# Optimization experiments

Hardware: AMD Instinct MI355X
Metric: run time of the kernel (lower is better)

The kernel has to match this reference:

```python
import jax, jax.numpy as jnp
import numpy as np

DK = 64

def setup_inputs() -> dict:
    key = jax.random.key(0)
    kx, kq, kk, kv = jax.random.split(key, 4)
    B, T, DM, DV = 256, 256, 384, 64
    x = jax.random.normal(kx, (B, T, DM), dtype=jnp.float32)
    s = 1.0 / np.sqrt(DM)
    W_q = jax.random.normal(kq, (DM, DK), dtype=jnp.float32) * s
    W_k = jax.random.normal(kk, (DM, DK), dtype=jnp.float32) * s
    W_v = jax.random.normal(kv, (DM, DV), dtype=jnp.float32) * s
    return {"x": x, "W_q": W_q, "W_k": W_k, "W_v": W_v}

def reference(x, W_q, W_k, W_v):
    # x: [B, T, dm]; projections to [B, T, dk]/[B, T, dv]
    q = jnp.einsum('btc,ck->btk', x, W_q)
    k = jnp.einsum('btc,ck->btk', x, W_k)
    v = jnp.einsum('btc,cv->btv', x, W_v)
    scale = k.shape[-1] ** (-0.5)
    wei = jnp.einsum('btk,bsk->bts', q, k) * scale  # [B, T, T]
    T = x.shape[1]
    causal = jnp.tril(jnp.ones((T, T), dtype=bool))
    wei = jnp.where(causal, wei, -jnp.inf)
    wei = jax.nn.softmax(wei, axis=-1)
    # dropout omitted (eval mode / deterministic reference)
    out = jnp.einsum('bts,bsv->btv', wei, v)
    return out
```

## Files before the change

### kernel.cpp

```cpp
#include <hip/hip_runtime.h>


typedef __attribute__((ext_vector_type(8))) short short8;
typedef __attribute__((ext_vector_type(4))) float floatx4;

__device__ inline unsigned short f2bf(float f) {
  union { float f; unsigned u; } v; v.f = f;
  unsigned r = v.u + 0x7FFFu + ((v.u >> 16) & 1u);
  return (unsigned short)(r >> 16);
}

__device__ inline void glds16(const void* g, void* l) {
  __builtin_amdgcn_global_load_lds(
      (const __attribute__((address_space(1))) void*)g,
      (__attribute__((address_space(3))) void*)l, 16, 0, 0);
}

__global__ void wt_kernel(const float* __restrict__ wq, const float* __restrict__ wk,
                          const float* __restrict__ wv, unsigned short* __restrict__ wt) {
  int idx = blockIdx.x * 256 + threadIdx.x;
  if (idx >= 3 * 64 * 384) return;
  int mat = idx / (64 * 384);
  int rem = idx % (64 * 384);
  int n = rem / 384, k = rem % 384;
  const float* w = (mat == 0) ? wq : ((mat == 1) ? wk : wv);
  wt[idx] = f2bf(w[k * 64 + n]);
}

__global__ __launch_bounds__(1024) void fused_kernel(
    const float* __restrict__ x, const unsigned short* __restrict__ wt,
    float* __restrict__ out) {
  __shared__ __align__(16) unsigned short wb[2][3 * 192 * 32];
  __shared__ __align__(16) unsigned short sK[256 * 72];
  __shared__ __align__(16) unsigned short sVT[64 * 264];

  int tid = threadIdx.x, lane = tid & 63, w = tid >> 6;
  int m = lane & 15, q = lane >> 4;
  int b = blockIdx.x;
  const float* xb = x + (size_t)b * 256 * 384;

  auto stage = [&](int mega, int buf) {
#pragma unroll
    for (int t = 0; t < 3; ++t) {
      int i = w + 16 * t;
      if (i < 36) {
        int kc = i / 12, sub = i % 12;
        int c = sub * 16 + (lane >> 2), g = lane & 3;
        glds16(wt + (size_t)c * 384 + (mega * 3 + kc) * 32 + g * 8,
               (void*)&wb[buf][kc * 6144 + sub * 512]);
      }
    }
  };

  floatx4 z = {0.f, 0.f, 0.f, 0.f};
  floatx4 acc[12];
#pragma unroll
  for (int nt = 0; nt < 12; ++nt) acc[nt] = z;

  stage(0, 0);
#pragma unroll
  for (int mega = 0; mega < 4; ++mega) {
    int buf = mega & 1;
    __syncthreads();
    if (mega < 3) stage(mega + 1, buf ^ 1);

#pragma unroll
    for (int kc = 0; kc < 3; ++kc) {
      int ks = mega * 3 + kc;
      const float* ap = xb + (size_t)(w * 16 + m) * 384 + ks * 32 + q * 8;
      float4 f0 = *(const float4*)ap;
      float4 f1 = *(const float4*)(ap + 4);
      short8 af;
      af[0] = (short)f2bf(f0.x); af[1] = (short)f2bf(f0.y);
      af[2] = (short)f2bf(f0.z); af[3] = (short)f2bf(f0.w);
      af[4] = (short)f2bf(f1.x); af[5] = (short)f2bf(f1.y);
      af[6] = (short)f2bf(f1.z); af[7] = (short)f2bf(f1.w);

      const unsigned short* wbk = &wb[buf][kc * 6144];
#pragma unroll
      for (int nt = 0; nt < 12; ++nt) {
        short8 bf = *(const short8*)&wbk[(nt * 16 + m) * 32 + q * 8];
        acc[nt] = __builtin_amdgcn_mfma_f32_16x16x32_bf16(af, bf, acc[nt], 0, 0, 0);
      }
    }
  }

  unsigned short* scr = &wb[0][0] + w * 1152;
#pragma unroll
  for (int nt = 0; nt < 8; ++nt) {
#pragma unroll
    for (int j = 0; j < 4; ++j) {
      unsigned short val = f2bf(acc[nt][j]);
      int lrow = q * 4 + j;
      if (nt < 4) scr[lrow * 72 + nt * 16 + m] = val;
      else        sK[(w * 16 + lrow) * 72 + (nt - 4) * 16 + m] = val;
    }
  }
#pragma unroll
  for (int nt = 8; nt < 12; ++nt) {
    ushort4 pv;
    pv.x = f2bf(acc[nt][0]); pv.y = f2bf(acc[nt][1]);
    pv.z = f2bf(acc[nt][2]); pv.w = f2bf(acc[nt][3]);
    *(ushort4*)&sVT[((nt - 8) * 16 + m) * 264 + w * 16 + q * 4] = pv;
  }

  short8 qf0 = *(const short8*)(scr + m * 72 + q * 8);
  short8 qf1 = *(const short8*)(scr + m * 72 + 32 + q * 8);

  __syncthreads();

  floatx4 sacc[16];
#pragma unroll
  for (int nt = 0; nt < 16; ++nt) {
    if (nt > w) continue;
    short8 kb0 = *(const short8*)(sK + (nt * 16 + m) * 72 + q * 8);
    short8 kb1 = *(const short8*)(sK + (nt * 16 + m) * 72 + 32 + q * 8);
    floatx4 t = __builtin_amdgcn_mfma_f32_16x16x32_bf16(qf0, kb0, z, 0, 0, 0);
    sacc[nt] = __builtin_amdgcn_mfma_f32_16x16x32_bf16(qf1, kb1, t, 0, 0, 0);
  }

  const float CSC = 0.18033688011112042f;
  float inv_[4];
  int rbase = w * 16 + q * 4;
#pragma unroll
  for (int j = 0; j < 4; ++j) {
    int rg = rbase + j;
    float sum = 0.f;
#pragma unroll
    for (int nt = 0; nt < 16; ++nt) {
      if (nt > w) continue;
      int col = nt * 16 + m;
      float p = (col <= rg) ? exp2f(sacc[nt][j] * CSC) : 0.f;
      sacc[nt][j] = p;
      sum += p;
    }
    sum += __shfl_xor(sum, 1);
    sum += __shfl_xor(sum, 2);
    sum += __shfl_xor(sum, 4);
    sum += __shfl_xor(sum, 8);
    inv_[j] = 1.f / sum;
  }

  floatx4 o[4];
#pragma unroll
  for (int vt = 0; vt < 4; ++vt) o[vt] = z;
#pragma unroll
  for (int c = 0; c < 4; ++c) {
    if (4 * c > w) continue;
#pragma unroll
    for (int t = 0; t < 4; ++t) {
      int nt = 4 * c + t;
#pragma unroll
      for (int j = 0; j < 4; ++j) {
        unsigned short pv = (nt <= w) ? f2bf(sacc[nt][j] * inv_[j]) : (unsigned short)0;
        scr[(q * 4 + j) * 72 + t * 16 + m] = pv;
      }
    }
    short8 pf0 = *(const short8*)(scr + m * 72 + q * 8);
    short8 pf1 = *(const short8*)(scr + m * 72 + 32 + q * 8);
#pragma unroll
    for (int vt = 0; vt < 4; ++vt) {
      short8 vb0 = *(const short8*)(sVT + (vt * 16 + m) * 264 + c * 64 + q * 8);
      short8 vb1 = *(const short8*)(sVT + (vt * 16 + m) * 264 + c * 64 + 32 + q * 8);
      o[vt] = __builtin_amdgcn_mfma_f32_16x16x32_bf16(pf0, vb0, o[vt], 0, 0, 0);
      o[vt] = __builtin_amdgcn_mfma_f32_16x16x32_bf16(pf1, vb1, o[vt], 0, 0, 0);
    }
  }

  float* op = out + ((size_t)b * 256 + w * 16) * 64;
#pragma unroll
  for (int vt = 0; vt < 4; ++vt)
#pragma unroll
    for (int j = 0; j < 4; ++j)
      op[(q * 4 + j) * 64 + vt * 16 + m] = o[vt][j];
}

extern "C" void kernel_launch(void* const* d_in, const int* in_sizes, int n_in,
                              void* d_out, int out_size, void* d_ws, size_t ws_size,
                              hipStream_t stream) {
  const float* x  = (const float*)d_in[0];
  const float* wq = (const float*)d_in[1];
  const float* wk = (const float*)d_in[2];
  const float* wv = (const float*)d_in[3];
  float* out = (float*)d_out;

  unsigned short* wt = (unsigned short*)d_ws;

  wt_kernel<<<288, 256, 0, stream>>>(wq, wk, wv, wt);
  fused_kernel<<<256, 1024, 0, stream>>>(x, wt, out);
}
```

Measured before the change: 170.8 us.

## Load all projection weights to LDS once and tile projection 2x6 per wave

The projection GEMM now stages the whole bf16 weight matrix (144KB) into LDS in a single pass, replacing the double-buffered staging with a sync per mega-step. Each wave computes a 32-row by 96-column tile instead of 16x192, so each weight fragment read from LDS feeds two MFMAs. The weight layout in LDS is XOR-swizzled to reduce bank conflicts. The x loads are software-prefetched one k-step ahead, and bf16 conversion uses packed intrinsics. Q now goes through a dedicated LDS region. The trade-off is a large LDS footprint and an upfront load that exposes the full weight fetch latency before any compute starts.

Result: slower. 176.2 us (+3.2%).

```diff
diff --git a/kernel.cpp b/kernel.cpp
--- a/kernel.cpp
+++ b/kernel.cpp
@@ -1,4 +1,5 @@
 #include <hip/hip_runtime.h>
+#include <hip/hip_bf16.h>
 
 
 typedef __attribute__((ext_vector_type(8))) short short8;
@@ -8,6 +9,11 @@
   union { float f; unsigned u; } v; v.f = f;
   unsigned r = v.u + 0x7FFFu + ((v.u >> 16) & 1u);
   return (unsigned short)(r >> 16);
+}
+__device__ inline unsigned pk2bf(float lo, float hi) {
+  __hip_bfloat162 h = __float22bfloat162_rn(make_float2(lo, hi));
+  union { __hip_bfloat162 h; unsigned u; } c; c.h = h;
+  return c.u;
 }
 
 __device__ inline void glds16(const void* g, void* l) {
@@ -30,85 +36,100 @@
 __global__ __launch_bounds__(1024) void fused_kernel(
     const float* __restrict__ x, const unsigned short* __restrict__ wt,
     float* __restrict__ out) {
-  __shared__ __align__(16) unsigned short wb[2][3 * 192 * 32];
-  __shared__ __align__(16) unsigned short sK[256 * 72];
-  __shared__ __align__(16) unsigned short sVT[64 * 264];
+  __shared__ __align__(16) unsigned char lds[147456];
+  unsigned short* wtl = (unsigned short*)lds;
+  unsigned short* sK  = (unsigned short*)lds;
+  unsigned short* sVT = (unsigned short*)(lds + 36864);
+  unsigned short* sQ  = (unsigned short*)(lds + 70656);
+  unsigned short* scrA = (unsigned short*)(lds + 107520);
 
   int tid = threadIdx.x, lane = tid & 63, w = tid >> 6;
   int m = lane & 15, q = lane >> 4;
+  int rg = w >> 1, cg = w & 1;
   int b = blockIdx.x;
   const float* xb = x + (size_t)b * 256 * 384;
 
-  auto stage = [&](int mega, int buf) {
-#pragma unroll
-    for (int t = 0; t < 3; ++t) {
-      int i = w + 16 * t;
-      if (i < 36) {
-        int kc = i / 12, sub = i % 12;
-        int c = sub * 16 + (lane >> 2), g = lane & 3;
-        glds16(wt + (size_t)c * 384 + (mega * 3 + kc) * 32 + g * 8,
-               (void*)&wb[buf][kc * 6144 + sub * 512]);
+#pragma unroll
+  for (int t = 0; t < 9; ++t) {
+    int i = w * 9 + t;
+    int chunk = i / 12, sub = i % 12;
+    int c = sub * 16 + (lane >> 2);
+    int g = (lane & 3) ^ (c & 3);
+    glds16(wt + (size_t)c * 384 + chunk * 32 + g * 8,
+           (void*)(wtl + i * 512));
+  }
+
+  const float* arow0 = xb + (size_t)(32 * rg + m) * 384 + q * 8;
+  const float* arow1 = arow0 + 16 * 384;
+  float4 c00 = *(const float4*)arow0, c01 = *(const float4*)(arow0 + 4);
+  float4 c10 = *(const float4*)arow1, c11 = *(const float4*)(arow1 + 4);
+
+  floatx4 z = {0.f, 0.f, 0.f, 0.f};
+  floatx4 acc[2][6];
+#pragma unroll
+  for (int a = 0; a < 2; ++a)
+#pragma unroll
+    for (int n = 0; n < 6; ++n) acc[a][n] = z;
+
+  __syncthreads();
+
+#pragma unroll 1
+  for (int ks = 0; ks < 12; ++ks) {
+    float4 n00, n01, n10, n11;
+    if (ks < 11) {
+      n00 = *(const float4*)(arow0 + (ks + 1) * 32);
+      n01 = *(const float4*)(arow0 + (ks + 1) * 32 + 4);
+      n10 = *(const float4*)(arow1 + (ks + 1) * 32);
+      n11 = *(const float4*)(arow1 + (ks + 1) * 32 + 4);
+    }
+    short8 af[2];
+    {
+      union { short8 s; unsigned u[4]; } t0, t1;
+      t0.u[0] = pk2bf(c00.x, c00.y); t0.u[1] = pk2bf(c00.z, c00.w);
+      t0.u[2] = pk2bf(c01.x, c01.y); t0.u[3] = pk2bf(c01.z, c01.w);
+      t1.u[0] = pk2bf(c10.x, c10.y); t1.u[1] = pk2bf(c10.z, c10.w);
+      t1.u[2] = pk2bf(c11.x, c11.y); t1.u[3] = pk2bf(c11.z, c11.w);
+      af[0] = t0.s; af[1] = t1.s;
+    }
+    const unsigned short* wck = wtl + ks * 6144;
+#pragma unroll
+    for (int nt = 0; nt < 6; ++nt) {
+      int c = cg * 96 + nt * 16 + m;
+      short8 bf = *(const short8*)&wck[c * 32 + (q ^ (m & 3)) * 8];
+      acc[0][nt] = __builtin_amdgcn_mfma_f32_16x16x32_bf16(af[0], bf, acc[0][nt], 0, 0, 0);
+      acc[1][nt] = __builtin_amdgcn_mfma_f32_16x16x32_bf16(af[1], bf, acc[1][nt], 0, 0, 0);
+    }
+    c00 = n00; c01 = n01; c10 = n10; c11 = n11;
+  }
+
+  __syncthreads();
+
+#pragma unroll
+  for (int mt = 0; mt < 2; ++mt) {
+    int rowb = 32 * rg + mt * 16 + q * 4;
+#pragma unroll
+    for (int nt = 0; nt < 6; ++nt) {
+      int cb = cg * 96 + nt * 16;
+      if (cb < 128) {
+#pragma unroll
+        for (int j = 0; j < 4; ++j) {
+          unsigned short val = f2bf(acc[mt][nt][j]);
+          if (cb < 64) sQ[(rowb + j) * 72 + cb + m]      = val;
+          else         sK[(rowb + j) * 72 + cb - 64 + m] = val;
+        }
+      } else {
+        ushort4 pv;
+        pv.x = f2bf(acc[mt][nt][0]); pv.y = f2bf(acc[mt][nt][1]);
+        pv.z = f2bf(acc[mt][nt][2]); pv.w = f2bf(acc[mt][nt][3]);
+        *(ushort4*)&sVT[(cb - 128 + m) * 264 + rowb] = pv;
       }
     }
-  };
-
-  floatx4 z = {0.f, 0.f, 0.f, 0.f};
-  floatx4 acc[12];
-#pragma unroll
-  for (int nt = 0; nt < 12; ++nt) acc[nt] = z;
-
-  stage(0, 0);
-#pragma unroll
-  for (int mega = 0; mega < 4; ++mega) {
-    int buf = mega & 1;
-    __syncthreads();
-    if (mega < 3) stage(mega + 1, buf ^ 1);
-
-#pragma unroll
-    for (int kc = 0; kc < 3; ++kc) {
-      int ks = mega * 3 + kc;
-      const float* ap = xb + (size_t)(w * 16 + m) * 384 + ks * 32 + q * 8;
-      float4 f0 = *(const float4*)ap;
-      float4 f1 = *(const float4*)(ap + 4);
-      short8 af;
-      af[0] = (short)f2bf(f0.x); af[1] = (short)f2bf(f0.y);
-      af[2] = (short)f2bf(f0.z); af[3] = (short)f2bf(f0.w);
-      af[4] = (short)f2bf(f1.x); af[5] = (short)f2bf(f1.y);
-      af[6] = (short)f2bf(f1.z); af[7] = (short)f2bf(f1.w);
-
-      const unsigned short* wbk = &wb[buf][kc * 6144];
-#pragma unroll
-      for (int nt = 0; nt < 12; ++nt) {
-        short8 bf = *(const short8*)&wbk[(nt * 16 + m) * 32 + q * 8];
-        acc[nt] = __builtin_amdgcn_mfma_f32_16x16x32_bf16(af, bf, acc[nt], 0, 0, 0);
-      }
-    }
-  }
-
-  unsigned short* scr = &wb[0][0] + w * 1152;
-#pragma unroll
-  for (int nt = 0; nt < 8; ++nt) {
-#pragma unroll
-    for (int j = 0; j < 4; ++j) {
-      unsigned short val = f2bf(acc[nt][j]);
-      int lrow = q * 4 + j;
-      if (nt < 4) scr[lrow * 72 + nt * 16 + m] = val;
-      else        sK[(w * 16 + lrow) * 72 + (nt - 4) * 16 + m] = val;
-    }
-  }
-#pragma unroll
-  for (int nt = 8; nt < 12; ++nt) {
-    ushort4 pv;
-    pv.x = f2bf(acc[nt][0]); pv.y = f2bf(acc[nt][1]);
-    pv.z = f2bf(acc[nt][2]); pv.w = f2bf(acc[nt][3]);
-    *(ushort4*)&sVT[((nt - 8) * 16 + m) * 264 + w * 16 + q * 4] = pv;
-  }
-
-  short8 qf0 = *(const short8*)(scr + m * 72 + q * 8);
-  short8 qf1 = *(const short8*)(scr + m * 72 + 32 + q * 8);
+  }
 
   __syncthreads();
 
+  short8 qf0 = *(const short8*)(sQ + (w * 16 + m) * 72 + q * 8);
+  short8 qf1 = *(const short8*)(sQ + (w * 16 + m) * 72 + 32 + q * 8);
   floatx4 sacc[16];
 #pragma unroll
   for (int nt = 0; nt < 16; ++nt) {
@@ -124,13 +145,13 @@
   int rbase = w * 16 + q * 4;
 #pragma unroll
   for (int j = 0; j < 4; ++j) {
-    int rg = rbase + j;
+    int rgl = rbase + j;
     float sum = 0.f;
 #pragma unroll
     for (int nt = 0; nt < 16; ++nt) {
       if (nt > w) continue;
       int col = nt * 16 + m;
-      float p = (col <= rg) ? exp2f(sacc[nt][j] * CSC) : 0.f;
+      float p = (col <= rgl) ? exp2f(sacc[nt][j] * CSC) : 0.f;
       sacc[nt][j] = p;
       sum += p;
     }
@@ -141,6 +162,7 @@
     inv_[j] = 1.f / sum;
   }
 
+  unsigned short* scr = scrA + w * 1152;
   floatx4 o[4];
 #pragma unroll
   for (int vt = 0; vt < 4; ++vt) o[vt] = z;
```
